# Kernel tuning notes

Measured on AMD Instinct MI355X. Metric: run time of the kernel, lower is better.

The kernel has to match this reference:

```python
import jax, jax.numpy as jnp
import numpy as np

HORIZON = 15
LAT = 6
CIN = 48  # input_dim // horizon
EPS = 1e-5
PAD = (HORIZON - 1) // 2  # 7


def _conv1d(x, w, b):
    # x: [B, Cin, L], w: [Cout, Cin, K], 'same' padding (pad=7, K=15)
    y = jax.lax.conv_general_dilated(
        x, w, window_strides=(1,), padding=[(PAD, PAD)],
        dimension_numbers=('NCH', 'OIH', 'NCH'))
    return y + b[None, :, None]


def _bn_ncl(x, g, b):
    # BatchNorm1d train-mode on [N, C, L]: stats over (N, L), biased var
    m = jnp.mean(x, axis=(0, 2), keepdims=True)
    v = jnp.mean(jnp.square(x - m), axis=(0, 2), keepdims=True)
    return (x - m) * jax.lax.rsqrt(v + EPS) * g[None, :, None] + b[None, :, None]


def setup_inputs() -> dict:
    key = jax.random.key(0)
    ks = jax.random.split(key, 16)
    B = 65536
    s1 = 1.0 / np.sqrt(CIN * HORIZON)
    s2 = 1.0 / np.sqrt(CIN * HORIZON)
    s3 = 1.0 / np.sqrt(2 * LAT * HORIZON)
    sp = 1.0 / np.sqrt(HORIZON)
    return {
        'x':  jax.random.normal(ks[0], (B, CIN * HORIZON), jnp.float32),
        'w1': jax.random.normal(ks[1], (CIN, CIN, HORIZON), jnp.float32) * s1,
        'b1': jax.random.normal(ks[2], (CIN,), jnp.float32) * s1,
        'g1': jnp.ones((CIN,), jnp.float32),
        'be1': jnp.zeros((CIN,), jnp.float32),
        'w2': jax.random.normal(ks[3], (2 * LAT, CIN, HORIZON), jnp.float32) * s2,
        'b2': jax.random.normal(ks[4], (2 * LAT,), jnp.float32) * s2,
        'g2': jnp.ones((2 * LAT,), jnp.float32),
        'be2': jnp.zeros((2 * LAT,), jnp.float32),
        'w3': jax.random.normal(ks[5], (LAT, 2 * LAT, HORIZON), jnp.float32) * s3,
        'b3': jax.random.normal(ks[6], (LAT,), jnp.float32) * s3,
        'pw': jax.random.normal(ks[7], (LAT, 2, HORIZON), jnp.float32) * sp,
        'pb': jax.random.normal(ks[8], (LAT, 2), jnp.float32) * sp,
        'pg': jnp.ones((LAT, 2), jnp.float32),
        'pbe': jnp.zeros((LAT, 2), jnp.float32),
    }


def reference(x, w1, b1, g1, be1, w2, b2, g2, be2, w3, b3, pw, pb, pg, pbe):
    B = x.shape[0]
    h = x.reshape(B, CIN, HORIZON)
    h = jax.nn.elu(_bn_ncl(_conv1d(h, w1, b1), g1, be1))
    h = jax.nn.elu(_bn_ncl(_conv1d(h, w2, b2), g2, be2))
    h = _conv1d(h, w3, b3)  # [B, LAT, HORIZON]

    # FFT spectral stats over last dim (length 15 -> 8 rfft bins)
    rf = jnp.fft.rfft(h, axis=2)
    power = jnp.square(jnp.abs(rf[:, :, 1:]))  # drop DC, [B, LAT, 7]
    freqs = jnp.arange(1, HORIZON // 2 + 1, dtype=h.dtype)  # rfftfreq(15)[1:]*15
    psum = jnp.sum(power, axis=2)
    f = jnp.sum(freqs * power, axis=2) / psum
    a = 2.0 * jnp.sqrt(psum) / HORIZON
    b_off = jnp.real(rf[:, :, 0]) / HORIZON

    # per-channel phase encoder, vectorized: Linear(15->2) + BatchNorm1d(2)
    v = jnp.einsum('bcl,col->bco', h, pw) + pb  # [B, LAT, 2]
    m = jnp.mean(v, axis=0, keepdims=True)
    var = jnp.mean(jnp.square(v - m), axis=0, keepdims=True)
    v = (v - m) * jax.lax.rsqrt(var + EPS) * pg + pbe
    p = jnp.arctan2(v[..., 1], v[..., 0]) / (2.0 * np.pi)  # [B, LAT]

    return jnp.concatenate([p, f, a, b_off], axis=-1)  # [B, 4*LAT]
```

## Files before the change

### kernel.cpp

```cpp
#include <hip/hip_runtime.h>
#include <math.h>

#define HORIZON 15
#define PAD 7
#define CIN 48
#define C2 12
#define LAT 6
#define EPS 1e-5f
#define NREP 16

typedef __bf16 bf16x8 __attribute__((ext_vector_type(8)));
typedef float f32x4 __attribute__((ext_vector_type(4)));
typedef unsigned short ushort8v __attribute__((ext_vector_type(8)));
typedef unsigned short ushortT;

__device__ inline void bfsplit(float v, ushortT& h, ushortT& l) {
    __bf16 bh = (__bf16)v;
    float fh = (float)bh;
    __bf16 bl = (__bf16)(v - fh);
    h = __builtin_bit_cast(ushortT, bh);
    l = __builtin_bit_cast(ushortT, bl);
}

__global__ void prep_kernel(const float* __restrict__ w1, const float* __restrict__ w2,
                            const float* __restrict__ w3,
                            ushortT* __restrict__ w1h, ushortT* __restrict__ w1l,
                            ushortT* __restrict__ w2h, ushortT* __restrict__ w2l,
                            float* __restrict__ w3t, float* __restrict__ trig) {
    int idx = blockIdx.x * blockDim.x + threadIdx.x;
    const int n1 = 768 * 736;
    const int n2 = 192 * 736;
    const int n3 = C2 * HORIZON * LAT;
    if (idx < n1) {
        int n = idx / 736, k = idx % 736;
        float v = 0.f;
        if (n < 720 && k < 720) {
            int l = n / 48, co = n % 48, ci = k / 15, t = k % 15;
            int d = t - l;
            if (d >= -PAD && d <= PAD) v = w1[(co * CIN + ci) * HORIZON + (d + PAD)];
        }
        ushortT h, lo; bfsplit(v, h, lo);
        w1h[idx] = h; w1l[idx] = lo;
    } else if (idx < n1 + n2) {
        int j = idx - n1;
        int n = j / 736, k = j % 736;
        float v = 0.f;
        if (n < 180 && k < 720) {
            int l = n / 12, co = n % 12, t = k / 48, ci = k % 48;
            int d = t - l;
            if (d >= -PAD && d <= PAD) v = w2[(co * CIN + ci) * HORIZON + (d + PAD)];
        }
        ushortT h, lo; bfsplit(v, h, lo);
        w2h[j] = h; w2l[j] = lo;
    } else if (idx < n1 + n2 + n3) {
        int j = idx - n1 - n2;
        int co = j % LAT; int r = j / LAT; int k = r % HORIZON; int ci = r / HORIZON;
        w3t[j] = w3[(co * C2 + ci) * HORIZON + k];
    } else if (idx < n1 + n2 + n3 + 7 * HORIZON) {
        int j = idx - (n1 + n2 + n3);
        int l = j % HORIZON; int f = j / HORIZON + 1;
        double ang = -2.0 * 3.14159265358979323846 * (double)(f * l) / 15.0;
        trig[j * 2]     = (float)cos(ang);
        trig[j * 2 + 1] = (float)sin(ang);
    }
}

template <int NFRAG, int CSTAT, bool FUSE_BN>
__global__ __launch_bounds__(256, 2)
void gemm_split(const float* __restrict__ A, int Ka,
                const ushortT* __restrict__ Bh, const ushortT* __restrict__ Bl,
                const float* __restrict__ bnp,
                float* __restrict__ Y, int ldy, int nreal,
                float* __restrict__ stats) {
    constexpr int NB = (NFRAG == 15) ? 16 : 12;
    __shared__ ushortT s_ah[8 * 512];
    __shared__ ushortT s_al[8 * 512];
    __shared__ ushortT s_bh[NB * 512];
    __shared__ ushortT s_bl[NB * 512];
    __shared__ float s_stats[2 * CSTAT];

    const int tid = threadIdx.x;
    const int w = tid >> 6, lane = tid & 63;
    const int lr = lane & 15, lq = lane >> 4;
    if (tid < 2 * CSTAT) s_stats[tid] = 0.f;

    const long m_base = (long)blockIdx.x * 128;
    const int n0 = blockIdx.y * (NFRAG * 16);

    f32x4 acc[2][NFRAG];
#pragma unroll
    for (int i = 0; i < 2; i++)
#pragma unroll
        for (int j = 0; j < NFRAG; j++) acc[i][j] = (f32x4){0.f, 0.f, 0.f, 0.f};

    const int KSTEPS = 736 / 32;
    for (int ks = 0; ks < KSTEPS; ks++) {
        const int k0 = ks * 32;
        __syncthreads();

#pragma unroll
        for (int j = 0; j < NB / 4; j++) {
            int nb = w * (NB / 4) + j;
            long grow = (long)(n0 + nb * 16 + lr) * 736 + k0 + lq * 8;
            ushort8v bvh = *(const ushort8v*)(Bh + grow);
            ushort8v bvl = *(const ushort8v*)(Bl + grow);
            *(ushort8v*)(s_bh + nb * 512 + lane * 8) = bvh;
            *(ushort8v*)(s_bl + nb * 512 + lane * 8) = bvl;
        }

#pragma unroll
        for (int j = 0; j < 2; j++) {
            int fb = w * 2 + j;
            long m = m_base + fb * 16 + lr;
            int k = k0 + lq * 8;
            ushort8v vh = (ushort8v)0, vl = (ushort8v)0;
            if (k < Ka) {
                const float4* p = (const float4*)(A + m * (long)Ka + k);
                float4 u0 = p[0], u1 = p[1];
                float f[8] = {u0.x, u0.y, u0.z, u0.w, u1.x, u1.y, u1.z, u1.w};
#pragma unroll
                for (int jj = 0; jj < 8; jj++) {
                    float v = f[jj];
                    if (FUSE_BN) {
                        int c = (k + jj) % 48;
                        float h = fmaf(v, bnp[c * 2], bnp[c * 2 + 1]);
                        v = h > 0.f ? h : expm1f(h);
                    }
                    ushortT hh, ll; bfsplit(v, hh, ll);
                    vh[jj] = hh; vl[jj] = ll;
                }
            }
            *(ushort8v*)(s_ah + fb * 512 + lane * 8) = vh;
            *(ushort8v*)(s_al + fb * 512 + lane * 8) = vl;
        }

        __syncthreads();

        bf16x8 ah[2], al[2];
#pragma unroll
        for (int fr = 0; fr < 2; fr++) {
            ah[fr] = *(const bf16x8*)(s_ah + (w * 2 + fr) * 512 + lane * 8);
            al[fr] = *(const bf16x8*)(s_al + (w * 2 + fr) * 512 + lane * 8);
        }
#pragma unroll
        for (int fc = 0; fc < NFRAG; fc++) {
            bf16x8 bhf = *(const bf16x8*)(s_bh + fc * 512 + lane * 8);
            bf16x8 blf = *(const bf16x8*)(s_bl + fc * 512 + lane * 8);
#pragma unroll
            for (int fr = 0; fr < 2; fr++) {
                acc[fr][fc] = __builtin_amdgcn_mfma_f32_16x16x32_bf16(ah[fr], bhf, acc[fr][fc], 0, 0, 0);
                acc[fr][fc] = __builtin_amdgcn_mfma_f32_16x16x32_bf16(al[fr], bhf, acc[fr][fc], 0, 0, 0);
                acc[fr][fc] = __builtin_amdgcn_mfma_f32_16x16x32_bf16(ah[fr], blf, acc[fr][fc], 0, 0, 0);
            }
        }
    }

    float ps[3] = {0.f, 0.f, 0.f}, qs[3] = {0.f, 0.f, 0.f};
#pragma unroll
    for (int fc = 0; fc < NFRAG; fc++) {
        int col = n0 + fc * 16 + lr;
        int j = fc % 3;
#pragma unroll
        for (int fr = 0; fr < 2; fr++) {
#pragma unroll
            for (int r = 0; r < 4; r++) {
                float v = acc[fr][fc][r];
                long row = m_base + w * 32 + fr * 16 + lq * 4 + r;
                if (col < nreal) Y[row * (long)ldy + col] = v;
                ps[j] += v;
                qs[j] = fmaf(v, v, qs[j]);
            }
        }
    }
#pragma unroll
    for (int j = 0; j < 3; j++) {
        int c = (lr + 16 * j) % CSTAT;
        atomicAdd(&s_stats[c], ps[j]);
        atomicAdd(&s_stats[CSTAT + c], qs[j]);
    }
    __syncthreads();
    if (tid < 2 * CSTAT)
        atomicAdd(&stats[(blockIdx.x & (NREP - 1)) * 2 * CSTAT + tid], s_stats[tid]);
}

__global__ void finalize_bn(const float* __restrict__ stats, const float* __restrict__ g,
                            const float* __restrict__ be, float* __restrict__ bn,
                            int C, float invN) {
    int c = threadIdx.x;
    if (c >= C) return;
    float s1 = 0.f, s2 = 0.f;
    for (int r = 0; r < NREP; r++) { s1 += stats[r * 2 * C + c]; s2 += stats[r * 2 * C + C + c]; }
    float m   = s1 * invN;
    float var = s2 * invN - m * m;
    float sc  = g[c] * rsqrtf(var + EPS);
    bn[c * 2]     = sc;
    bn[c * 2 + 1] = fmaf(-m, sc, be[c]);
}

__global__ __launch_bounds__(256) void tail_kernel(const float* __restrict__ h2,
                                                   const float* __restrict__ w3t,
                                                   const float* __restrict__ b3,
                                                   const float* __restrict__ pw,
                                                   const float* __restrict__ trig,
                                                   const float* __restrict__ bn2,
                                                   float* __restrict__ out,
                                                   float* __restrict__ vout,
                                                   float* __restrict__ stats) {
    __shared__ float s_sum[2 * LAT];
    __shared__ float s_sq[2 * LAT];
    int t = threadIdx.x;
    if (t < 2 * LAT) { s_sum[t] = 0.f; s_sq[t] = 0.f; }
    __syncthreads();

    int id = blockIdx.x * 256 + t;
    int co = id % LAT;
    long b = id / LAT;
    const float* xr = h2 + b * (long)(C2 * HORIZON);

    float acc[HORIZON];
#pragma unroll
    for (int l = 0; l < HORIZON; l++) acc[l] = b3[co];

    for (int ci = 0; ci < C2; ci++) {
        float sc = bn2[ci * 2], sh = bn2[ci * 2 + 1];
        float xv[HORIZON];
#pragma unroll
        for (int tt = 0; tt < HORIZON; tt++) {
            float h = fmaf(xr[tt * C2 + ci], sc, sh);
            xv[tt] = h > 0.f ? h : expm1f(h);
        }
        float wv[HORIZON];
#pragma unroll
        for (int k = 0; k < HORIZON; k++) wv[k] = w3t[(ci * HORIZON + k) * LAT + co];
#pragma unroll
        for (int tt = 0; tt < HORIZON; tt++) {
            const int lo = (tt - PAD) > 0 ? (tt - PAD) : 0;
            const int hi = (tt + PAD) < (HORIZON - 1) ? (tt + PAD) : (HORIZON - 1);
#pragma unroll
            for (int l = lo; l <= hi; l++)
                acc[l] = fmaf(xv[tt], wv[tt - l + PAD], acc[l]);
        }
    }

    float ssum = 0.f;
#pragma unroll
    for (int l = 0; l < HORIZON; l++) ssum += acc[l];
    float b_off = ssum * (1.f / 15.f);

    float psum = 0.f, fnum = 0.f;
#pragma unroll
    for (int j = 0; j < 7; j++) {
        float re = 0.f, im = 0.f;
#pragma unroll
        for (int l = 0; l < HORIZON; l++) {
            float c = trig[(j * HORIZON + l) * 2];
            float s = trig[(j * HORIZON + l) * 2 + 1];
            re = fmaf(acc[l], c, re);
            im = fmaf(acc[l], s, im);
        }
        float p = fmaf(re, re, im * im);
        psum += p;
        fnum = fmaf((float)(j + 1), p, fnum);
    }
    float f = fnum / psum;
    float a = 2.f * sqrtf(psum) * (1.f / 15.f);

    float* orow = out + b * 24;
    orow[6 + co]  = f;
    orow[12 + co] = a;
    orow[18 + co] = b_off;

    float v0 = 0.f, v1 = 0.f;
#pragma unroll
    for (int l = 0; l < HORIZON; l++) {
        v0 = fmaf(acc[l], pw[(co * 2 + 0) * HORIZON + l], v0);
        v1 = fmaf(acc[l], pw[(co * 2 + 1) * HORIZON + l], v1);
    }
    vout[b * 12 + co * 2]     = v0;
    vout[b * 12 + co * 2 + 1] = v1;
    atomicAdd(&s_sum[co * 2], v0);
    atomicAdd(&s_sq[co * 2], v0 * v0);
    atomicAdd(&s_sum[co * 2 + 1], v1);
    atomicAdd(&s_sq[co * 2 + 1], v1 * v1);

    __syncthreads();
    float* st = stats + (blockIdx.x & (NREP - 1)) * 2 * (2 * LAT);
    if (t < 2 * LAT) {
        atomicAdd(&st[t], s_sum[t]);
        atomicAdd(&st[2 * LAT + t], s_sq[t]);
    }
}

__global__ void phase_kernel(const float* __restrict__ v, const float* __restrict__ bnP,
                             float* __restrict__ out, long B) {
    long b = (long)blockIdx.x * 256 + threadIdx.x;
    if (b >= B) return;
#pragma unroll
    for (int co = 0; co < LAT; co++) {
        float v0 = v[b * 12 + co * 2];
        float v1 = v[b * 12 + co * 2 + 1];
        int c0 = co * 2, c1 = co * 2 + 1;
        v0 = fmaf(v0, bnP[c0 * 2], bnP[c0 * 2 + 1]);
        v1 = fmaf(v1, bnP[c1 * 2], bnP[c1 * 2 + 1]);
        out[b * 24 + co] = atan2f(v1, v0) * 0.15915494309189535f;
    }
}

extern "C" void kernel_launch(void* const* d_in, const int* in_sizes, int n_in,
                              void* d_out, int out_size, void* d_ws, size_t ws_size,
                              hipStream_t stream) {
    const float* x   = (const float*)d_in[0];
    const float* w1  = (const float*)d_in[1];
    const float* g1  = (const float*)d_in[3];
    const float* be1 = (const float*)d_in[4];
    const float* w2  = (const float*)d_in[5];
    const float* g2  = (const float*)d_in[7];
    const float* be2 = (const float*)d_in[8];
    const float* w3  = (const float*)d_in[9];
    const float* b3  = (const float*)d_in[10];
    const float* pw  = (const float*)d_in[11];
    const float* pg  = (const float*)d_in[13];
    const float* pbe = (const float*)d_in[14];
    float* out = (float*)d_out;

    long B = (long)in_sizes[0] / (CIN * HORIZON);

    ushortT* w1h = (ushortT*)d_ws;
    ushortT* w1l = w1h + 768 * 736;
    ushortT* w2h = w1l + 768 * 736;
    ushortT* w2l = w2h + 192 * 736;
    float* y1 = (float*)(w2l + 192 * 736);
    float* y2 = y1 + B * 720;
    float* vv = y2 + B * 180;
    float* stats1 = vv + B * 12;
    float* stats2 = stats1 + NREP * 96;
    float* statsP = stats2 + NREP * 24;
    float* bn1 = statsP + NREP * 24;
    float* bn2 = bn1 + 96;
    float* bnP = bn2 + 24;
    float* w3t = bnP + 24;
    float* trig = w3t + C2 * HORIZON * LAT;

    hipMemsetAsync(stats1, 0, NREP * (96 + 24 + 24) * sizeof(float), stream);

    const int prep_total = 768 * 736 + 192 * 736 + C2 * HORIZON * LAT + 7 * HORIZON;
    prep_kernel<<<(prep_total + 255) / 256, 256, 0, stream>>>(w1, w2, w3, w1h, w1l, w2h, w2l, w3t, trig);

    gemm_split<15, 48, false><<<dim3((int)(B / 128), 3), 256, 0, stream>>>(
        x, 720, w1h, w1l, nullptr, y1, 720, 720, stats1);
    finalize_bn<<<1, 64, 0, stream>>>(stats1, g1, be1, bn1, CIN, 1.f / (float)(B * HORIZON));

    gemm_split<12, 12, true><<<dim3((int)(B / 128), 1), 256, 0, stream>>>(
        y1, 720, w2h, w2l, bn1, y2, 180, 180, stats2);
    finalize_bn<<<1, 64, 0, stream>>>(stats2, g2, be2, bn2, C2, 1.f / (float)(B * HORIZON));

    tail_kernel<<<(int)(B * LAT / 256), 256, 0, stream>>>(y2, w3t, b3, pw, trig, bn2, out, vv, statsP);
    finalize_bn<<<1, 64, 0, stream>>>(statsP, pg, pbe, bnP, 2 * LAT, 1.f / (float)B);

    phase_kernel<<<(int)((B + 255) / 256), 256, 0, stream>>>(vv, bnP, out, B);
}
```

Measured before the change: 773.8 us.

## Double-buffer GEMM k-loop with direct global-to-LDS loads and register A split

Rewrites the split-bf16 GEMM main loop as a two-stage software pipeline: B tiles go straight from global memory into double-buffered LDS through global_load_lds, and A tiles are prefetched into registers one step ahead and split into hi/lo bf16 in registers rather than staged through LDS. It also caches the BN scale/shift in LDS, raises wave priority around the MFMA block, and swaps the grid axes so the N-tile blocks sharing an A row are launched next to each other, which should improve A reuse in L2. The aim is to hide global-load latency behind MFMA work and remove LDS round trips for A. The cost is more register pressure, which may hurt occupancy at two blocks per SM, and a hand-written vmcnt count that has to stay exactly in step with the issued loads.

```diff
diff --git a/kernel.cpp b/kernel.cpp
--- a/kernel.cpp
+++ b/kernel.cpp
@@ -65,6 +65,12 @@
     }
 }
 
+#define SBAR() asm volatile("s_barrier" ::: "memory")
+#define GLDS16(SRC, DST)                                                      \
+    __builtin_amdgcn_global_load_lds(                                         \
+        (const __attribute__((address_space(1))) void*)(SRC),                 \
+        (__attribute__((address_space(3))) void*)(DST), 16, 0, 0)
+
 template <int NFRAG, int CSTAT, bool FUSE_BN>
 __global__ __launch_bounds__(256, 2)
 void gemm_split(const float* __restrict__ A, int Ka,
@@ -72,88 +78,145 @@
                 const float* __restrict__ bnp,
                 float* __restrict__ Y, int ldy, int nreal,
                 float* __restrict__ stats) {
-    constexpr int NB = (NFRAG == 15) ? 16 : 12;
-    __shared__ ushortT s_ah[8 * 512];
-    __shared__ ushortT s_al[8 * 512];
-    __shared__ ushortT s_bh[NB * 512];
-    __shared__ ushortT s_bl[NB * 512];
+    constexpr int NB  = (NFRAG == 15) ? 16 : 12;
+    constexpr int NBW = NB / 4;
+    constexpr int NVM = NBW * 2 + 4;
+
+    __shared__ __attribute__((aligned(16))) ushortT s_bh[2][NB * 512];
+    __shared__ __attribute__((aligned(16))) ushortT s_bl[2][NB * 512];
     __shared__ float s_stats[2 * CSTAT];
+    __shared__ float s_bnp[96];
 
     const int tid = threadIdx.x;
     const int w = tid >> 6, lane = tid & 63;
     const int lr = lane & 15, lq = lane >> 4;
     if (tid < 2 * CSTAT) s_stats[tid] = 0.f;
-
-    const long m_base = (long)blockIdx.x * 128;
-    const int n0 = blockIdx.y * (NFRAG * 16);
+    if (FUSE_BN && tid < 96) s_bnp[tid] = bnp[tid];
+    __syncthreads();
+
+    const long m_base = (long)blockIdx.y * 128;
+    const int n0 = blockIdx.x * (NFRAG * 16);
+
+    const float* arow0 = A + (m_base + w * 32 + lr) * (long)Ka;
+    const float* arow1 = arow0 + 16 * (long)Ka;
+    const long bdelta = Bl - Bh;
+    const ushortT* bsrc[NBW];
+#pragma unroll
+    for (int j = 0; j < NBW; j++)
+        bsrc[j] = Bh + (long)(n0 + (w * NBW + j) * 16 + lr) * 736 + lq * 8;
 
     f32x4 acc[2][NFRAG];
 #pragma unroll
     for (int i = 0; i < 2; i++)
 #pragma unroll
-        for (int j = 0; j < NFRAG; j++) acc[i][j] = (f32x4){0.f, 0.f, 0.f, 0.f};
-
-    const int KSTEPS = 736 / 32;
-    for (int ks = 0; ks < KSTEPS; ks++) {
-        const int k0 = ks * 32;
-        __syncthreads();
-
-#pragma unroll
-        for (int j = 0; j < NB / 4; j++) {
-            int nb = w * (NB / 4) + j;
-            long grow = (long)(n0 + nb * 16 + lr) * 736 + k0 + lq * 8;
-            ushort8v bvh = *(const ushort8v*)(Bh + grow);
-            ushort8v bvl = *(const ushort8v*)(Bl + grow);
-            *(ushort8v*)(s_bh + nb * 512 + lane * 8) = bvh;
-            *(ushort8v*)(s_bl + nb * 512 + lane * 8) = bvl;
-        }
-
-#pragma unroll
-        for (int j = 0; j < 2; j++) {
-            int fb = w * 2 + j;
-            long m = m_base + fb * 16 + lr;
-            int k = k0 + lq * 8;
-            ushort8v vh = (ushort8v)0, vl = (ushort8v)0;
-            if (k < Ka) {
-                const float4* p = (const float4*)(A + m * (long)Ka + k);
-                float4 u0 = p[0], u1 = p[1];
-                float f[8] = {u0.x, u0.y, u0.z, u0.w, u1.x, u1.y, u1.z, u1.w};
-#pragma unroll
-                for (int jj = 0; jj < 8; jj++) {
-                    float v = f[jj];
-                    if (FUSE_BN) {
-                        int c = (k + jj) % 48;
-                        float h = fmaf(v, bnp[c * 2], bnp[c * 2 + 1]);
-                        v = h > 0.f ? h : expm1f(h);
-                    }
-                    ushortT hh, ll; bfsplit(v, hh, ll);
-                    vh[jj] = hh; vl[jj] = ll;
-                }
-            }
-            *(ushort8v*)(s_ah + fb * 512 + lane * 8) = vh;
-            *(ushort8v*)(s_al + fb * 512 + lane * 8) = vl;
-        }
-
-        __syncthreads();
-
-        bf16x8 ah[2], al[2];
-#pragma unroll
-        for (int fr = 0; fr < 2; fr++) {
-            ah[fr] = *(const bf16x8*)(s_ah + (w * 2 + fr) * 512 + lane * 8);
-            al[fr] = *(const bf16x8*)(s_al + (w * 2 + fr) * 512 + lane * 8);
-        }
-#pragma unroll
-        for (int fc = 0; fc < NFRAG; fc++) {
-            bf16x8 bhf = *(const bf16x8*)(s_bh + fc * 512 + lane * 8);
-            bf16x8 blf = *(const bf16x8*)(s_bl + fc * 512 + lane * 8);
-#pragma unroll
-            for (int fr = 0; fr < 2; fr++) {
-                acc[fr][fc] = __builtin_amdgcn_mfma_f32_16x16x32_bf16(ah[fr], bhf, acc[fr][fc], 0, 0, 0);
-                acc[fr][fc] = __builtin_amdgcn_mfma_f32_16x16x32_bf16(al[fr], bhf, acc[fr][fc], 0, 0, 0);
-                acc[fr][fc] = __builtin_amdgcn_mfma_f32_16x16x32_bf16(ah[fr], blf, acc[fr][fc], 0, 0, 0);
-            }
-        }
-    }
+        for (int jf = 0; jf < NFRAG; jf++) acc[i][jf] = (f32x4){0.f, 0.f, 0.f, 0.f};
+
+    float4 pfA[4], pfB[4];
+    bf16x8 ah[2], al[2];
+
+#define ISSUE_STEP(KS, BUF, PF)                                               \
+    do {                                                                      \
+        const int k0_ = (KS) * 32;                                            \
+        _Pragma("unroll")                                                     \
+        for (int j_ = 0; j_ < NBW; j_++) {                                    \
+            const ushortT* g_ = bsrc[j_] + k0_;                               \
+            GLDS16(g_, &s_bh[BUF][(w * NBW + j_) * 512]);                     \
+            GLDS16(g_ + bdelta, &s_bl[BUF][(w * NBW + j_) * 512]);            \
+        }                                                                     \
+        const int ka_ = k0_ + lq * 8;                                         \
+        _Pragma("unroll")                                                     \
+        for (int fr_ = 0; fr_ < 2; fr_++) {                                   \
+            float4 z_ = make_float4(0.f, 0.f, 0.f, 0.f);                      \
+            PF[fr_ * 2] = z_; PF[fr_ * 2 + 1] = z_;                           \
+            if (ka_ < Ka) {                                                   \
+                const float4* p_ =                                            \
+                    (const float4*)((fr_ ? arow1 : arow0) + ka_);             \
+                PF[fr_ * 2] = p_[0]; PF[fr_ * 2 + 1] = p_[1];                 \
+            }                                                                 \
+        }                                                                     \
+    } while (0)
+
+#define SPLIT_STEP(PF, KS)                                                    \
+    do {                                                                      \
+        const int kb_ = (KS) * 32 + lq * 8;                                   \
+        float4 qq_[4];                                                        \
+        if (FUSE_BN) {                                                        \
+            const int cb_ = (kb_ % 48) * 2;       \
+            _Pragma("unroll")                                                 \
+            for (int m_ = 0; m_ < 4; m_++)                                    \
+                qq_[m_] = *(const float4*)(&s_bnp[cb_ + m_ * 4]);             \
+        }                                                                     \
+        _Pragma("unroll")                                                     \
+        for (int fr_ = 0; fr_ < 2; fr_++) {                                   \
+            float f_[8] = {PF[fr_*2].x,   PF[fr_*2].y,                        \
+                           PF[fr_*2].z,   PF[fr_*2].w,                        \
+                           PF[fr_*2+1].x, PF[fr_*2+1].y,                      \
+                           PF[fr_*2+1].z, PF[fr_*2+1].w};                     \
+            ushort8v uh_, ul_;                                                \
+            _Pragma("unroll")                                                 \
+            for (int jj = 0; jj < 8; jj++) {                                  \
+                float v_ = f_[jj];                                            \
+                if (FUSE_BN) {                                                \
+                    float sc_ = (jj & 1) ? qq_[jj >> 1].z : qq_[jj >> 1].x;   \
+                    float sh_ = (jj & 1) ? qq_[jj >> 1].w : qq_[jj >> 1].y;   \
+                    float h_ = fmaf(v_, sc_, sh_);                            \
+                    v_ = h_ > 0.f ? h_ : expm1f(h_);                          \
+                }                                                             \
+                ushortT hh_, ll_; bfsplit(v_, hh_, ll_);                      \
+                uh_[jj] = hh_; ul_[jj] = ll_;                                 \
+            }                                                                 \
+            ah[fr_] = __builtin_bit_cast(bf16x8, uh_);                        \
+            al[fr_] = __builtin_bit_cast(bf16x8, ul_);                        \
+        }                                                                     \
+    } while (0)
+
+#define COMPUTE_STEP(BUF)                                                     \
+    do {                                                                      \
+        __builtin_amdgcn_s_setprio(1);                                        \
+        _Pragma("unroll")                                                     \
+        for (int fc = 0; fc < NFRAG; fc++) {                                  \
+            bf16x8 bhf = *(const bf16x8*)(&s_bh[BUF][fc * 512 + lane * 8]);   \
+            bf16x8 blf = *(const bf16x8*)(&s_bl[BUF][fc * 512 + lane * 8]);   \
+            _Pragma("unroll")                                                 \
+            for (int fr = 0; fr < 2; fr++) {                                  \
+                acc[fr][fc] = __builtin_amdgcn_mfma_f32_16x16x32_bf16(        \
+                    ah[fr], bhf, acc[fr][fc], 0, 0, 0);                       \
+                acc[fr][fc] = __builtin_amdgcn_mfma_f32_16x16x32_bf16(        \
+                    al[fr], bhf, acc[fr][fc], 0, 0, 0);                       \
+                acc[fr][fc] = __builtin_amdgcn_mfma_f32_16x16x32_bf16(        \
+                    ah[fr], blf, acc[fr][fc], 0, 0, 0);                       \
+            }                                                                 \
+        }                                                                     \
+        __builtin_amdgcn_s_setprio(0);                                        \
+    } while (0)
+
+#define WAITP() asm volatile("s_waitcnt vmcnt(%0)" ::"n"(NVM) : "memory")
+
+    ISSUE_STEP(0, 0, pfA);
+#pragma unroll 1
+    for (int k2 = 0; k2 + 2 < 23; k2 += 2) {
+        ISSUE_STEP(k2 + 1, 1, pfB);
+        WAITP();
+        SBAR();
+        SPLIT_STEP(pfA, k2);
+        COMPUTE_STEP(0);
+        SBAR();
+        ISSUE_STEP(k2 + 2, 0, pfA);
+        WAITP();
+        SBAR();
+        SPLIT_STEP(pfB, k2 + 1);
+        COMPUTE_STEP(1);
+        SBAR();
+    }
+    asm volatile("s_waitcnt vmcnt(0)" ::: "memory");
+    SBAR();
+    SPLIT_STEP(pfA, 22);
+    COMPUTE_STEP(0);
+
+#undef ISSUE_STEP
+#undef SPLIT_STEP
+#undef COMPUTE_STEP
+#undef WAITP
 
     float ps[3] = {0.f, 0.f, 0.f}, qs[3] = {0.f, 0.f, 0.f};
 #pragma unroll
@@ -180,7 +243,7 @@
     }
     __syncthreads();
     if (tid < 2 * CSTAT)
-        atomicAdd(&stats[(blockIdx.x & (NREP - 1)) * 2 * CSTAT + tid], s_stats[tid]);
+        atomicAdd(&stats[(blockIdx.y & (NREP - 1)) * 2 * CSTAT + tid], s_stats[tid]);
 }
 
 __global__ void finalize_bn(const float* __restrict__ stats, const float* __restrict__ g,
@@ -346,11 +409,11 @@
     const int prep_total = 768 * 736 + 192 * 736 + C2 * HORIZON * LAT + 7 * HORIZON;
     prep_kernel<<<(prep_total + 255) / 256, 256, 0, stream>>>(w1, w2, w3, w1h, w1l, w2h, w2l, w3t, trig);
 
-    gemm_split<15, 48, false><<<dim3((int)(B / 128), 3), 256, 0, stream>>>(
+    gemm_split<15, 48, false><<<dim3(3, (int)(B / 128)), 256, 0, stream>>>(
         x, 720, w1h, w1l, nullptr, y1, 720, 720, stats1);
     finalize_bn<<<1, 64, 0, stream>>>(stats1, g1, be1, bn1, CIN, 1.f / (float)(B * HORIZON));
 
-    gemm_split<12, 12, true><<<dim3((int)(B / 128), 1), 256, 0, stream>>>(
+    gemm_split<12, 12, true><<<dim3(1, (int)(B / 128)), 256, 0, stream>>>(
         y1, 720, w2h, w2l, bn1, y2, 180, 180, stats2);
     finalize_bn<<<1, 64, 0, stream>>>(stats2, g2, be2, bn2, C2, 1.f / (float)(B * HORIZON));
 
```

After: 721.8 us. -6.7%, faster.

## Pre-split activations to bf16 pairs and double-buffer GEMM with direct-to-LDS loads

Applied to the files above, without the earlier changes.

Moves the fp32-to-bf16 hi/lo split, and for the second layer the BN+ELU, out of the GEMM inner loop into separate elementwise kernels that write bf16 pairs to workspace. The GEMM becomes a double-buffered pipeline using global_load_lds, explicit vmcnt waits and raw barriers, with raised priority around the MFMA block. Blocks are remapped so row blocks stay grouped per XCD, with smaller column tiles (8 and 6 fragments). This trades extra global traffic for the split buffers and two more launches against a shorter, overlapped GEMM main loop.

```diff
diff --git a/kernel.cpp b/kernel.cpp
--- a/kernel.cpp
+++ b/kernel.cpp
@@ -29,7 +29,7 @@
                             float* __restrict__ w3t, float* __restrict__ trig) {
     int idx = blockIdx.x * blockDim.x + threadIdx.x;
     const int n1 = 768 * 736;
-    const int n2 = 192 * 736;
+    const int n2 = 256 * 736;
     const int n3 = C2 * HORIZON * LAT;
     if (idx < n1) {
         int n = idx / 736, k = idx % 736;
@@ -65,100 +65,175 @@
     }
 }
 
-template <int NFRAG, int CSTAT, bool FUSE_BN>
+__global__ __launch_bounds__(256) void split_x_kernel(const float* __restrict__ in,
+                                                      ushortT* __restrict__ oh,
+                                                      ushortT* __restrict__ ol, long n) {
+    long i = ((long)blockIdx.x * 256 + threadIdx.x) * 8;
+    if (i >= n) return;
+    float4 u0 = *(const float4*)(in + i);
+    float4 u1 = *(const float4*)(in + i + 4);
+    float f[8] = {u0.x, u0.y, u0.z, u0.w, u1.x, u1.y, u1.z, u1.w};
+    ushort8v h, l;
+#pragma unroll
+    for (int j = 0; j < 8; j++) { ushortT hh, ll; bfsplit(f[j], hh, ll); h[j] = hh; l[j] = ll; }
+    *(ushort8v*)(oh + i) = h;
+    *(ushort8v*)(ol + i) = l;
+    if (i == 0) {
+#pragma unroll
+        for (int j = 0; j < 32; j++) { oh[n + j] = 0; ol[n + j] = 0; }
+    }
+}
+
+__global__ __launch_bounds__(256) void split_bn_kernel(const float* __restrict__ in,
+                                                       const float* __restrict__ bn,
+                                                       ushortT* __restrict__ oh,
+                                                       ushortT* __restrict__ ol, long n) {
+    long i = ((long)blockIdx.x * 256 + threadIdx.x) * 8;
+    if (i >= n) return;
+    const int c0 = (int)(i % 48);
+    float4 q[4];
+#pragma unroll
+    for (int m = 0; m < 4; m++) q[m] = *(const float4*)(bn + c0 * 2 + m * 4);
+    float4 u0 = *(const float4*)(in + i);
+    float4 u1 = *(const float4*)(in + i + 4);
+    float f[8] = {u0.x, u0.y, u0.z, u0.w, u1.x, u1.y, u1.z, u1.w};
+    ushort8v h, l;
+#pragma unroll
+    for (int j = 0; j < 8; j++) {
+        float sc = (j & 1) ? q[j >> 1].z : q[j >> 1].x;
+        float sh = (j & 1) ? q[j >> 1].w : q[j >> 1].y;
+        float hv = fmaf(f[j], sc, sh);
+        float v = hv > 0.f ? hv : expm1f(hv);
+        ushortT hh, ll; bfsplit(v, hh, ll); h[j] = hh; l[j] = ll;
+    }
+    *(ushort8v*)(oh + i) = h;
+    *(ushort8v*)(ol + i) = l;
+    if (i == 0) {
+#pragma unroll
+        for (int j = 0; j < 32; j++) { oh[n + j] = 0; ol[n + j] = 0; }
+    }
+}
+
+#define SBAR() asm volatile("s_barrier" ::: "memory")
+#define WAITN(N) asm volatile("s_waitcnt vmcnt(" #N ")" ::: "memory")
+#define GLDS16(SRC, DST)                                                      \
+    __builtin_amdgcn_global_load_lds(                                         \
+        (const __attribute__((address_space(1))) void*)(SRC),                 \
+        (__attribute__((address_space(3))) void*)(DST), 16, 0, 0)
+
+template <int NFRAG, int CSTAT, int NCG>
 __global__ __launch_bounds__(256, 2)
-void gemm_split(const float* __restrict__ A, int Ka,
-                const ushortT* __restrict__ Bh, const ushortT* __restrict__ Bl,
-                const float* __restrict__ bnp,
-                float* __restrict__ Y, int ldy, int nreal,
-                float* __restrict__ stats) {
-    constexpr int NB = (NFRAG == 15) ? 16 : 12;
-    __shared__ ushortT s_ah[8 * 512];
-    __shared__ ushortT s_al[8 * 512];
-    __shared__ ushortT s_bh[NB * 512];
-    __shared__ ushortT s_bl[NB * 512];
+void gemm_bf16(const ushortT* __restrict__ Ah, const ushortT* __restrict__ Al,
+               const ushortT* __restrict__ Bh, const ushortT* __restrict__ Bl,
+               float* __restrict__ Y, int ldy, int nreal,
+               float* __restrict__ stats) {
+    __shared__ __attribute__((aligned(16))) ushortT s_a[2][2][4096];
+    __shared__ __attribute__((aligned(16))) ushortT s_b[2][2][4096];
     __shared__ float s_stats[2 * CSTAT];
 
     const int tid = threadIdx.x;
     const int w = tid >> 6, lane = tid & 63;
     const int lr = lane & 15, lq = lane >> 4;
     if (tid < 2 * CSTAT) s_stats[tid] = 0.f;
-
-    const long m_base = (long)blockIdx.x * 128;
-    const int n0 = blockIdx.y * (NFRAG * 16);
+    __syncthreads();
+
+    const int bid = blockIdx.x;
+    const int xcd = bid & 7, s = bid >> 3;
+    const int rpx = (gridDim.x >> 3) / NCG;
+    const int col = s % NCG;
+    const int rowblk = xcd * rpx + s / NCG;
+    const long m_base = (long)rowblk * 128;
+    const int n0 = col * (NFRAG * 16);
+
+    const ushortT* asrc = Ah + (m_base + w * 32 + (lane >> 2)) * 720L + (lane & 3) * 8;
+    const long adelta = Al - Ah;
+    const ushortT* bsrc[2];
+#pragma unroll
+    for (int j = 0; j < 2; j++)
+        bsrc[j] = Bh + (long)(n0 + (w * 2 + j) * 16 + lr) * 736 + lq * 8;
+    const long bdelta = Bl - Bh;
 
     f32x4 acc[2][NFRAG];
 #pragma unroll
     for (int i = 0; i < 2; i++)
 #pragma unroll
-        for (int j = 0; j < NFRAG; j++) acc[i][j] = (f32x4){0.f, 0.f, 0.f, 0.f};
-
-    const int KSTEPS = 736 / 32;
-    for (int ks = 0; ks < KSTEPS; ks++) {
-        const int k0 = ks * 32;
-        __syncthreads();
-
-#pragma unroll
-        for (int j = 0; j < NB / 4; j++) {
-            int nb = w * (NB / 4) + j;
-            long grow = (long)(n0 + nb * 16 + lr) * 736 + k0 + lq * 8;
-            ushort8v bvh = *(const ushort8v*)(Bh + grow);
-            ushort8v bvl = *(const ushort8v*)(Bl + grow);
-            *(ushort8v*)(s_bh + nb * 512 + lane * 8) = bvh;
-            *(ushort8v*)(s_bl + nb * 512 + lane * 8) = bvl;
-        }
-
-#pragma unroll
-        for (int j = 0; j < 2; j++) {
-            int fb = w * 2 + j;
-            long m = m_base + fb * 16 + lr;
-            int k = k0 + lq * 8;
-            ushort8v vh = (ushort8v)0, vl = (ushort8v)0;
-            if (k < Ka) {
-                const float4* p = (const float4*)(A + m * (long)Ka + k);
-                float4 u0 = p[0], u1 = p[1];
-                float f[8] = {u0.x, u0.y, u0.z, u0.w, u1.x, u1.y, u1.z, u1.w};
-#pragma unroll
-                for (int jj = 0; jj < 8; jj++) {
-                    float v = f[jj];
-                    if (FUSE_BN) {
-                        int c = (k + jj) % 48;
-                        float h = fmaf(v, bnp[c * 2], bnp[c * 2 + 1]);
-                        v = h > 0.f ? h : expm1f(h);
-                    }
-                    ushortT hh, ll; bfsplit(v, hh, ll);
-                    vh[jj] = hh; vl[jj] = ll;
-                }
-            }
-            *(ushort8v*)(s_ah + fb * 512 + lane * 8) = vh;
-            *(ushort8v*)(s_al + fb * 512 + lane * 8) = vl;
-        }
-
-        __syncthreads();
-
-        bf16x8 ah[2], al[2];
-#pragma unroll
-        for (int fr = 0; fr < 2; fr++) {
-            ah[fr] = *(const bf16x8*)(s_ah + (w * 2 + fr) * 512 + lane * 8);
-            al[fr] = *(const bf16x8*)(s_al + (w * 2 + fr) * 512 + lane * 8);
-        }
-#pragma unroll
-        for (int fc = 0; fc < NFRAG; fc++) {
-            bf16x8 bhf = *(const bf16x8*)(s_bh + fc * 512 + lane * 8);
-            bf16x8 blf = *(const bf16x8*)(s_bl + fc * 512 + lane * 8);
-#pragma unroll
-            for (int fr = 0; fr < 2; fr++) {
-                acc[fr][fc] = __builtin_amdgcn_mfma_f32_16x16x32_bf16(ah[fr], bhf, acc[fr][fc], 0, 0, 0);
-                acc[fr][fc] = __builtin_amdgcn_mfma_f32_16x16x32_bf16(al[fr], bhf, acc[fr][fc], 0, 0, 0);
-                acc[fr][fc] = __builtin_amdgcn_mfma_f32_16x16x32_bf16(ah[fr], blf, acc[fr][fc], 0, 0, 0);
-            }
-        }
-    }
+        for (int jf = 0; jf < NFRAG; jf++) acc[i][jf] = (f32x4){0.f, 0.f, 0.f, 0.f};
+
+#define ISSUE(KS, BUF)                                                        \
+    do {                                                                      \
+        const long k0_ = (KS) * 32;                                           \
+        _Pragma("unroll")                                                     \
+        for (int j_ = 0; j_ < 2; j_++) {                                      \
+            const ushortT* g_ = bsrc[j_] + k0_;                               \
+            GLDS16(g_, &s_b[BUF][0][(w * 2 + j_) * 512]);                     \
+            GLDS16(g_ + bdelta, &s_b[BUF][1][(w * 2 + j_) * 512]);            \
+        }                                                                     \
+        _Pragma("unroll")                                                     \
+        for (int d_ = 0; d_ < 2; d_++) {                                      \
+            const ushortT* g_ = asrc + d_ * (16 * 720L) + k0_;                \
+            GLDS16(g_, &s_a[BUF][0][w * 1024 + d_ * 512]);                    \
+            GLDS16(g_ + adelta, &s_a[BUF][1][w * 1024 + d_ * 512]);           \
+        }                                                                     \
+    } while (0)
+
+#define COMPUTE(BUF)                                                          \
+    do {                                                                      \
+        const int af_ = w * 1024 + (lr * 4 + lq) * 8;                         \
+        bf16x8 ah0 = *(const bf16x8*)(&s_a[BUF][0][af_]);                     \
+        bf16x8 ah1 = *(const bf16x8*)(&s_a[BUF][0][af_ + 512]);               \
+        bf16x8 al0 = *(const bf16x8*)(&s_a[BUF][1][af_]);                     \
+        bf16x8 al1 = *(const bf16x8*)(&s_a[BUF][1][af_ + 512]);               \
+        __builtin_amdgcn_s_setprio(1);                                        \
+        _Pragma("unroll")                                                     \
+        for (int fc = 0; fc < NFRAG; fc++) {                                  \
+            bf16x8 bhf = *(const bf16x8*)(&s_b[BUF][0][fc * 512 + lane * 8]); \
+            bf16x8 blf = *(const bf16x8*)(&s_b[BUF][1][fc * 512 + lane * 8]); \
+            acc[0][fc] = __builtin_amdgcn_mfma_f32_16x16x32_bf16(             \
+                ah0, bhf, acc[0][fc], 0, 0, 0);                               \
+            acc[0][fc] = __builtin_amdgcn_mfma_f32_16x16x32_bf16(             \
+                al0, bhf, acc[0][fc], 0, 0, 0);                               \
+            acc[0][fc] = __builtin_amdgcn_mfma_f32_16x16x32_bf16(             \
+                ah0, blf, acc[0][fc], 0, 0, 0);                               \
+            acc[1][fc] = __builtin_amdgcn_mfma_f32_16x16x32_bf16(             \
+                ah1, bhf, acc[1][fc], 0, 0, 0);                               \
+            acc[1][fc] = __builtin_amdgcn_mfma_f32_16x16x32_bf16(             \
+                al1, bhf, acc[1][fc], 0, 0, 0);                               \
+            acc[1][fc] = __builtin_amdgcn_mfma_f32_16x16x32_bf16(             \
+                ah1, blf, acc[1][fc], 0, 0, 0);                               \
+        }                                                                     \
+        __builtin_amdgcn_s_setprio(0);                                        \
+    } while (0)
+
+    ISSUE(0, 0);
+    ISSUE(1, 1);
+#pragma unroll 1
+    for (int k2 = 0; k2 < 20; k2 += 2) {
+        WAITN(8); SBAR();
+        COMPUTE(0);
+        SBAR();
+        ISSUE(k2 + 2, 0);
+        WAITN(8); SBAR();
+        COMPUTE(1);
+        SBAR();
+        ISSUE(k2 + 3, 1);
+    }
+    WAITN(8); SBAR();
+    COMPUTE(0);
+    SBAR();
+    ISSUE(22, 0);
+    WAITN(8); SBAR();
+    COMPUTE(1);
+    SBAR();
+    WAITN(0); SBAR();
+    COMPUTE(0);
+
+#undef ISSUE
+#undef COMPUTE
 
     float ps[3] = {0.f, 0.f, 0.f}, qs[3] = {0.f, 0.f, 0.f};
 #pragma unroll
     for (int fc = 0; fc < NFRAG; fc++) {
-        int col = n0 + fc * 16 + lr;
+        int colY = n0 + fc * 16 + lr;
         int j = fc % 3;
 #pragma unroll
         for (int fr = 0; fr < 2; fr++) {
@@ -166,7 +241,7 @@
             for (int r = 0; r < 4; r++) {
                 float v = acc[fr][fc][r];
                 long row = m_base + w * 32 + fr * 16 + lq * 4 + r;
-                if (col < nreal) Y[row * (long)ldy + col] = v;
+                if (colY < nreal) Y[row * (long)ldy + colY] = v;
                 ps[j] += v;
                 qs[j] = fmaf(v, v, qs[j]);
             }
@@ -174,13 +249,13 @@
     }
 #pragma unroll
     for (int j = 0; j < 3; j++) {
-        int c = (lr + 16 * j) % CSTAT;
+        int c = (n0 + lr + 16 * j) % CSTAT;
         atomicAdd(&s_stats[c], ps[j]);
         atomicAdd(&s_stats[CSTAT + c], qs[j]);
     }
     __syncthreads();
     if (tid < 2 * CSTAT)
-        atomicAdd(&stats[(blockIdx.x & (NREP - 1)) * 2 * CSTAT + tid], s_stats[tid]);
+        atomicAdd(&stats[(rowblk & (NREP - 1)) * 2 * CSTAT + tid], s_stats[tid]);
 }
 
 __global__ void finalize_bn(const float* __restrict__ stats, const float* __restrict__ g,
@@ -324,13 +399,16 @@
     float* out = (float*)d_out;
 
     long B = (long)in_sizes[0] / (CIN * HORIZON);
+    const long NA = B * 720;
 
     ushortT* w1h = (ushortT*)d_ws;
     ushortT* w1l = w1h + 768 * 736;
     ushortT* w2h = w1l + 768 * 736;
-    ushortT* w2l = w2h + 192 * 736;
-    float* y1 = (float*)(w2l + 192 * 736);
-    float* y2 = y1 + B * 720;
+    ushortT* w2l = w2h + 256 * 736;
+    ushortT* xh  = w2l + 256 * 736;
+    ushortT* xl  = xh + (NA + 32);
+    float* y1 = (float*)(xl + (NA + 32));
+    float* y2 = y1 + NA;
     float* vv = y2 + B * 180;
     float* stats1 = vv + B * 12;
     float* stats2 = stats1 + NREP * 96;
@@ -343,15 +421,19 @@
 
     hipMemsetAsync(stats1, 0, NREP * (96 + 24 + 24) * sizeof(float), stream);
 
-    const int prep_total = 768 * 736 + 192 * 736 + C2 * HORIZON * LAT + 7 * HORIZON;
+    const int prep_total = 768 * 736 + 256 * 736 + C2 * HORIZON * LAT + 7 * HORIZON;
     prep_kernel<<<(prep_total + 255) / 256, 256, 0, stream>>>(w1, w2, w3, w1h, w1l, w2h, w2l, w3t, trig);
 
-    gemm_split<15, 48, false><<<dim3((int)(B / 128), 3), 256, 0, stream>>>(
-        x, 720, w1h, w1l, nullptr, y1, 720, 720, stats1);
+    split_x_kernel<<<(int)(NA / 8 / 256), 256, 0, stream>>>(x, xh, xl, NA);
+
+    gemm_bf16<8, 48, 6><<<3072, 256, 0, stream>>>(
+        xh, xl, w1h, w1l, y1, 720, 720, stats1);
     finalize_bn<<<1, 64, 0, stream>>>(stats1, g1, be1, bn1, CIN, 1.f / (float)(B * HORIZON));
 
-    gemm_split<12, 12, true><<<dim3((int)(B / 128), 1), 256, 0, stream>>>(
-        y1, 720, w2h, w2l, bn1, y2, 180, 180, stats2);
+    split_bn_kernel<<<(int)(NA / 8 / 256), 256, 0, stream>>>(y1, bn1, xh, xl, NA);
+
+    gemm_bf16<6, 12, 2><<<1024, 256, 0, stream>>>(
+        xh, xl, w2h, w2l, y2, 180, 180, stats2);
     finalize_bn<<<1, 64, 0, stream>>>(stats2, g2, be2, bn2, C2, 1.f / (float)(B * HORIZON));
 
     tail_kernel<<<(int)(B * LAT / 256), 256, 0, stream>>>(y2, w3t, b3, pw, trig, bn2, out, vv, statsP);
```

Result: slower. 959.5 us (+24.0%).
